# Optimization experiments

Hardware: AMD Instinct MI355X
Metric: run time of the kernel (lower is better)

The kernel has to match this reference:

```python
import jax, jax.numpy as jnp
import numpy as np

D_MODEL = 1024
N_HEADS = 16
HEAD_DIM = D_MODEL // N_HEADS
NEG = -10000.0  # module uses -10000, not -inf


def setup_inputs() -> dict:
    key = jax.random.key(0)
    ks = jax.random.split(key, 8)
    B, T = 4, 2048
    q = jax.random.normal(ks[0], (B, T, D_MODEL), dtype=jnp.float32)
    k = jax.random.normal(ks[1], (B, T, D_MODEL), dtype=jnp.float32)
    v = jax.random.normal(ks[2], (B, T, D_MODEL), dtype=jnp.float32)
    attn_mask = jnp.ones((B, T), dtype=jnp.float32)
    # xavier_uniform for square [d, d] weights: limit = sqrt(6/(d+d))
    lim = float(np.sqrt(6.0 / (D_MODEL + D_MODEL)))
    Wq = jax.random.uniform(ks[3], (D_MODEL, D_MODEL), jnp.float32, -lim, lim)
    Wk = jax.random.uniform(ks[4], (D_MODEL, D_MODEL), jnp.float32, -lim, lim)
    Wv = jax.random.uniform(ks[5], (D_MODEL, D_MODEL), jnp.float32, -lim, lim)
    Wo = jax.random.uniform(ks[6], (D_MODEL, D_MODEL), jnp.float32, -lim, lim)
    return {"q": q, "k": k, "v": v, "attn_mask": attn_mask,
            "Wq": Wq, "Wk": Wk, "Wv": Wv, "Wo": Wo, "mask_future": 1}


def _split_heads(x):
    B, T, _ = x.shape
    return x.reshape(B, T, N_HEADS, HEAD_DIM).transpose(0, 2, 1, 3)  # [B,H,T,D]


def reference(q, k, v, attn_mask, Wq, Wk, Wv, Wo, mask_future):
    # torch Linear: y = x @ W.T  (weights stored [out, in])
    qh = _split_heads(jnp.einsum('btd,ed->bte', q, Wq))
    kh = _split_heads(jnp.einsum('btd,ed->bte', k, Wk))
    vh = _split_heads(jnp.einsum('btd,ed->bte', v, Wv))
    L, S = qh.shape[-2], kh.shape[-2]
    # dual scale: each of q and k scaled by 1/d**0.25
    scale = 1.0 / jnp.sqrt(jnp.sqrt(jnp.float32(HEAD_DIM)))
    scores = jnp.einsum('bhld,bhsd->bhls', qh * scale, kh * scale)
    if mask_future:
        causal_bias = jnp.triu(jnp.full((L, S), NEG, dtype=scores.dtype), k=1)
        scores = scores + causal_bias
    # padding mask: attn_mask [B, S] -> broadcast [B,1,1,S]; 0 entries -> -10000
    pad = attn_mask[:, None, None, :]
    scores = jnp.where(pad == 0, jnp.asarray(NEG, scores.dtype), scores)
    probs = jax.nn.softmax(scores, axis=-1)  # dropout p=0.0 -> identity
    ctx = jnp.einsum('bhls,bhsd->bhld', probs, vh)
    B = ctx.shape[0]
    ctx = ctx.transpose(0, 2, 1, 3).reshape(B, L, D_MODEL)
    return jnp.einsum('btd,ed->bte', ctx, Wo)
```

## Files before the change

### kernel.cpp

```cpp
#include <hip/hip_runtime.h>

typedef unsigned short u16;
typedef __attribute__((ext_vector_type(8))) __bf16 bf16x8;
typedef __attribute__((ext_vector_type(4))) float f32x4;

#define T_SEQ 2048
#define NH 16
#define DH 64
#define DM 1024
#define NEG2 (-14426.95f)
#define QS2 (0.42466089f)

__device__ __forceinline__ u16 f2bf(float x) {
  union { float f; unsigned u; } c; c.f = x;
  unsigned r = c.u + 0x7fffu + ((c.u >> 16) & 1u);
  return (u16)(r >> 16);
}

__device__ __forceinline__ void async_load16(const void* g, void* l) {
  __builtin_amdgcn_global_load_lds(
      (const __attribute__((address_space(1))) unsigned int*)(g),
      (__attribute__((address_space(3))) unsigned int*)(l), 16, 0, 0);
}

__global__ __launch_bounds__(256) void convert_all(
    const float* __restrict__ q, const float* __restrict__ k, const float* __restrict__ v,
    const float* __restrict__ Wq, const float* __restrict__ Wk, const float* __restrict__ Wv,
    const float* __restrict__ Wo, u16* __restrict__ xb, u16* __restrict__ wb) {
  int blk = blockIdx.x;
  const float* src; u16* dst;
  if (blk < 12288) {
    int s = blk >> 12;
    src = (s == 0) ? q : (s == 1) ? k : v;
    dst = xb + (size_t)s * 8388608u;
    blk &= 4095;
  } else {
    int s = (blk - 12288) >> 9;
    src = (s == 0) ? Wq : (s == 1) ? Wk : (s == 2) ? Wv : Wo;
    dst = wb + (size_t)s * 1048576u;
    blk = (blk - 12288) & 511;
  }
  size_t base = (size_t)blk * 2048 + (size_t)threadIdx.x * 8;
  float4 a = *(const float4*)(src + base);
  float4 b2 = *(const float4*)(src + base + 4);
  u16 o[8] __attribute__((aligned(16)));
  o[0] = f2bf(a.x); o[1] = f2bf(a.y); o[2] = f2bf(a.z); o[3] = f2bf(a.w);
  o[4] = f2bf(b2.x); o[5] = f2bf(b2.y); o[6] = f2bf(b2.z); o[7] = f2bf(b2.w);
  *(uint4*)(dst + base) = *(const uint4*)o;
}

__global__ __launch_bounds__(256) void gemm_qkv(const u16* __restrict__ A,
                                                const u16* __restrict__ Wqb,
                                                const u16* __restrict__ Wkb,
                                                const u16* __restrict__ Wvb,
                                                u16* __restrict__ Qh, u16* __restrict__ Kh,
                                                u16* __restrict__ VTh) {
  __shared__ char lds[32768];
  const int tid = threadIdx.x;
  const int wid = tid >> 6, lane = tid & 63;
  const int lm = lane & 15, lq = lane >> 4;
  const int m0 = blockIdx.x * 128;
  const int n0 = blockIdx.y * 128;
  const int which = n0 >> 10;
  const int n0l = n0 & 1023;
  const u16* As = A + (size_t)which * 8388608u;
  const u16* Bw = (which == 0) ? Wqb : (which == 1) ? Wkb : Wvb;
  const int wm = wid >> 1, wn = wid & 1;
  f32x4 acc[4][4] = {};

  for (int kt = 0; kt < 1024; kt += 64) {
    __syncthreads();
    for (int i = 0; i < 4; ++i) {
      int p = wid * 4 + i;
      int mt = p >> 1, kk = p & 1;
      int col = kt + kk * 32 + lq * 8;
      async_load16(As + (size_t)(m0 + mt * 16 + lm) * 1024 + col, lds + p * 1024);
      async_load16(Bw + (size_t)(n0l + mt * 16 + lm) * 1024 + col, lds + 16384 + p * 1024);
    }
    __syncthreads();
    for (int kk = 0; kk < 2; ++kk) {
      bf16x8 af[4], bf[4];
      for (int i = 0; i < 4; ++i) {
        af[i] = *(const bf16x8*)(lds + ((wm * 4 + i) * 2 + kk) * 1024 + lane * 16);
        bf[i] = *(const bf16x8*)(lds + 16384 + ((wn * 4 + i) * 2 + kk) * 1024 + lane * 16);
      }
      for (int i = 0; i < 4; ++i)
        for (int j = 0; j < 4; ++j)
          acc[i][j] = __builtin_amdgcn_mfma_f32_16x16x32_bf16(af[i], bf[j], acc[i][j], 0, 0, 0);
    }
  }

  if (which < 2) {
    u16* O = which ? Kh : Qh;
    for (int i = 0; i < 4; ++i) {
      int row = m0 + wm * 64 + i * 16 + lq * 4;
      for (int j = 0; j < 4; ++j) {
        int nc = n0l + wn * 64 + j * 16 + lm;
        int h = nc >> 6, dh = nc & 63;
        for (int r = 0; r < 4; ++r) {
          int m = row + r;
          int b = m >> 11, t = m & 2047;
          O[(((size_t)(b * NH + h) * T_SEQ + t) << 6) + dh] = f2bf(acc[i][j][r] * QS2);
        }
      }
    }
  } else {
    for (int i = 0; i < 4; ++i) {
      int row = m0 + wm * 64 + i * 16 + lq * 4;
      int b = row >> 11, t0 = row & 2047;
      for (int j = 0; j < 4; ++j) {
        int nc = n0l + wn * 64 + j * 16 + lm;
        int h = nc >> 6, dh = nc & 63;
        u16 tmp[4] __attribute__((aligned(8)));
        for (int r = 0; r < 4; ++r) tmp[r] = f2bf(acc[i][j][r]);
        *(uint2*)(VTh + (((size_t)(b * NH + h) * DH + dh) << 11) + t0) = *(const uint2*)tmp;
      }
    }
  }
}

__global__ __launch_bounds__(256) void gemm_out(const u16* __restrict__ A,
                                                const u16* __restrict__ Bw,
                                                float* __restrict__ O) {
  __shared__ char lds[32768];
  const int tid = threadIdx.x;
  const int wid = tid >> 6, lane = tid & 63;
  const int lm = lane & 15, lq = lane >> 4;
  const int m0 = blockIdx.x * 128, n0 = blockIdx.y * 128;
  const int wm = wid >> 1, wn = wid & 1;
  f32x4 acc[4][4] = {};

  for (int kt = 0; kt < 1024; kt += 64) {
    __syncthreads();
    for (int i = 0; i < 4; ++i) {
      int p = wid * 4 + i;
      int mt = p >> 1, kk = p & 1;
      int col = kt + kk * 32 + lq * 8;
      async_load16(A + (size_t)(m0 + mt * 16 + lm) * 1024 + col, lds + p * 1024);
      async_load16(Bw + (size_t)(n0 + mt * 16 + lm) * 1024 + col, lds + 16384 + p * 1024);
    }
    __syncthreads();
    for (int kk = 0; kk < 2; ++kk) {
      bf16x8 af[4], bf[4];
      for (int i = 0; i < 4; ++i) {
        af[i] = *(const bf16x8*)(lds + ((wm * 4 + i) * 2 + kk) * 1024 + lane * 16);
        bf[i] = *(const bf16x8*)(lds + 16384 + ((wn * 4 + i) * 2 + kk) * 1024 + lane * 16);
      }
      for (int i = 0; i < 4; ++i)
        for (int j = 0; j < 4; ++j)
          acc[i][j] = __builtin_amdgcn_mfma_f32_16x16x32_bf16(af[i], bf[j], acc[i][j], 0, 0, 0);
    }
  }
  for (int i = 0; i < 4; ++i) {
    int row = m0 + wm * 64 + i * 16 + lq * 4;
    for (int j = 0; j < 4; ++j) {
      int col = n0 + wn * 64 + j * 16 + lm;
      for (int r = 0; r < 4; ++r)
        O[(size_t)(row + r) * 1024 + col] = acc[i][j][r];
    }
  }
}

__global__ __launch_bounds__(256) void attn_kernel(const u16* __restrict__ Qh,
                                                   const u16* __restrict__ Kh,
                                                   const u16* __restrict__ VTh,
                                                   const float* __restrict__ attn_mask,
                                                   const int* __restrict__ mfp,
                                                   u16* __restrict__ ctx) {
  __shared__ char kls[8192];
  __shared__ char vls[8192];
  __shared__ char pls[4][2048];
  __shared__ float maskb[T_SEQ];

  const int tid = threadIdx.x;
  const int wid = tid >> 6, lane = tid & 63;
  const int lm = lane & 15, lq = lane >> 4;
  const int bid = blockIdx.x;
  const int pr = bid & 15, h = (bid >> 4) & 15, b = bid >> 8;
  const int mf = *mfp;
  const size_t bh = (size_t)(b * NH + h);
  const u16* Qbh = Qh + bh * T_SEQ * DH;
  const u16* Kbh = Kh + bh * T_SEQ * DH;
  const u16* VTbh = VTh + bh * DH * T_SEQ;

  for (int i = tid; i < T_SEQ; i += 256)
    maskb[i] = (attn_mask[(size_t)b * T_SEQ + i] == 0.0f) ? NEG2 : 0.0f;

  for (int half = 0; half < 2; ++half) {
    const int qt = half ? (31 - pr) : pr;
    const int q0 = qt * 64;
    const int qw = q0 + wid * 16;
    bf16x8 qf[2];
    qf[0] = *(const bf16x8*)(Qbh + (size_t)(qw + lm) * DH + lq * 8);
    qf[1] = *(const bf16x8*)(Qbh + (size_t)(qw + lm) * DH + 32 + lq * 8);

    f32x4 acc[4] = {};
    float mprev = -1e30f, lsum = 0.f;

    const int nch = mf ? (qt + 1) : 32;
    for (int c = 0; c < nch; ++c) {
      const int s0 = c * 64;
      __syncthreads();
      async_load16(Kbh + (size_t)(s0 + wid * 16 + lm) * DH + lq * 8, kls + (wid * 2 + 0) * 1024);
      async_load16(Kbh + (size_t)(s0 + wid * 16 + lm) * DH + 32 + lq * 8, kls + (wid * 2 + 1) * 1024);
      async_load16(VTbh + (size_t)(wid * 16 + lm) * T_SEQ + s0 + lq * 8, vls + (wid * 2 + 0) * 1024);
      async_load16(VTbh + (size_t)(wid * 16 + lm) * T_SEQ + s0 + 32 + lq * 8, vls + (wid * 2 + 1) * 1024);
      __syncthreads();

      f32x4 sc[4];
      for (int st = 0; st < 4; ++st) {
        f32x4 z = {0.f, 0.f, 0.f, 0.f};
        sc[st] = z;
        for (int kk = 0; kk < 2; ++kk) {
          bf16x8 kf = *(const bf16x8*)(kls + ((st * 2 + kk) * 64 + lane) * 16);
          sc[st] = __builtin_amdgcn_mfma_f32_16x16x32_bf16(kf, qf[kk], sc[st], 0, 0, 0);
        }
      }
      for (int st = 0; st < 4; ++st) {
        f32x4 mb = *(const f32x4*)(maskb + s0 + st * 16 + lq * 4);
        for (int r = 0; r < 4; ++r) sc[st][r] += mb[r];
      }
      if (mf && (s0 + 64 > qw)) {
        int qg = qw + lm;
        for (int st = 0; st < 4; ++st)
          for (int r = 0; r < 4; ++r)
            if (s0 + st * 16 + lq * 4 + r > qg) sc[st][r] = NEG2;
      }
      float mx = fmaxf(fmaxf(sc[0][0], sc[0][1]), fmaxf(sc[0][2], sc[0][3]));
      for (int st = 1; st < 4; ++st) {
        float t2 = fmaxf(fmaxf(sc[st][0], sc[st][1]), fmaxf(sc[st][2], sc[st][3]));
        mx = fmaxf(mx, t2);
      }
      mx = fmaxf(mx, __shfl_xor(mx, 16));
      mx = fmaxf(mx, __shfl_xor(mx, 32));
      float mn = fmaxf(mprev, mx);
      float alpha = exp2f(mprev - mn);
      float ps = 0.f;
      for (int st = 0; st < 4; ++st)
        for (int r = 0; r < 4; ++r) {
          float p = exp2f(sc[st][r] - mn);
          sc[st][r] = p;
          ps += p;
        }
      ps += __shfl_xor(ps, 16);
      ps += __shfl_xor(ps, 32);
      lsum = lsum * alpha + ps;
      mprev = mn;
      for (int r = 0; r < 4; ++r) {
        float ar = __shfl(alpha, lq * 4 + r);
        for (int nt = 0; nt < 4; ++nt) acc[nt][r] *= ar;
      }
      {
        char* pw = pls[wid];
        for (int st = 0; st < 4; ++st) {
          int kk = st >> 1;
          int lqp = (st & 1) * 2 + (lq >> 1);
          int base = kk * 1024 + (lqp * 16 + lm) * 16 + (lq & 1) * 8;
          unsigned v0 = (unsigned)f2bf(sc[st][0]) | ((unsigned)f2bf(sc[st][1]) << 16);
          unsigned v1 = (unsigned)f2bf(sc[st][2]) | ((unsigned)f2bf(sc[st][3]) << 16);
          *(unsigned*)(pw + base) = v0;
          *(unsigned*)(pw + base + 4) = v1;
        }
      }
      asm volatile("s_waitcnt lgkmcnt(0)" ::: "memory");
      for (int kk = 0; kk < 2; ++kk) {
        bf16x8 pf = *(const bf16x8*)(pls[wid] + kk * 1024 + lane * 16);
        for (int nt = 0; nt < 4; ++nt) {
          bf16x8 vf = *(const bf16x8*)(vls + ((nt * 2 + kk) * 64 + lane) * 16);
          acc[nt] = __builtin_amdgcn_mfma_f32_16x16x32_bf16(pf, vf, acc[nt], 0, 0, 0);
        }
      }
    }
    float inv = 1.0f / lsum;
    for (int r = 0; r < 4; ++r) {
      float ir = __shfl(inv, lq * 4 + r);
      int t = qw + lq * 4 + r;
      for (int nt = 0; nt < 4; ++nt)
        ctx[((size_t)(b * T_SEQ + t) * DM) + h * DH + nt * 16 + lm] = f2bf(acc[nt][r] * ir);
    }
  }
}

extern "C" void kernel_launch(void* const* d_in, const int* in_sizes, int n_in,
                              void* d_out, int out_size, void* d_ws, size_t ws_size,
                              hipStream_t stream) {
  const float* q = (const float*)d_in[0];
  const float* k = (const float*)d_in[1];
  const float* v = (const float*)d_in[2];
  const float* attn_mask = (const float*)d_in[3];
  const float* Wq = (const float*)d_in[4];
  const float* Wk = (const float*)d_in[5];
  const float* Wv = (const float*)d_in[6];
  const float* Wo = (const float*)d_in[7];
  const int* mf = (const int*)d_in[8];

  u16* ws = (u16*)d_ws;
  u16* qb  = ws;
  u16* wqb = ws + 3u * 8388608u;
  u16* wkb = wqb + 1048576u;
  u16* wvb = wkb + 1048576u;
  u16* wob = wvb + 1048576u;
  u16* Qh  = wob + 1048576u;
  u16* Kh  = Qh + 8388608u;
  u16* VTh = Kh + 8388608u;
  u16* ctxb = ws;

  convert_all<<<14336, 256, 0, stream>>>(q, k, v, Wq, Wk, Wv, Wo, qb, wqb);

  dim3 gq(64, 24);
  gemm_qkv<<<gq, 256, 0, stream>>>(qb, wqb, wkb, wvb, Qh, Kh, VTh);

  attn_kernel<<<1024, 256, 0, stream>>>(Qh, Kh, VTh, attn_mask, mf, ctxb);

  dim3 gg(64, 8);
  gemm_out<<<gg, 256, 0, stream>>>(ctxb, wob, (float*)d_out);
}
```

Measured before the change: 399.0 us.

## Switch to fp16 MFMA, stage QKV epilogue via LDS, skip unused mask and rescale

```diff
diff --git a/kernel.cpp b/kernel.cpp
--- a/kernel.cpp
+++ b/kernel.cpp
@@ -1,7 +1,8 @@
 #include <hip/hip_runtime.h>
 
 typedef unsigned short u16;
-typedef __attribute__((ext_vector_type(8))) __bf16 bf16x8;
+typedef __attribute__((ext_vector_type(8))) _Float16 f16x8;
+typedef __attribute__((ext_vector_type(2))) __fp16 fp16v2;
 typedef __attribute__((ext_vector_type(4))) float f32x4;
 
 #define T_SEQ 2048
@@ -11,10 +12,13 @@
 #define NEG2 (-14426.95f)
 #define QS2 (0.42466089f)
 
-__device__ __forceinline__ u16 f2bf(float x) {
-  union { float f; unsigned u; } c; c.f = x;
-  unsigned r = c.u + 0x7fffu + ((c.u >> 16) & 1u);
-  return (u16)(r >> 16);
+__device__ __forceinline__ unsigned pk2(float a, float b) {
+  union { fp16v2 v; unsigned u; } c;
+  c.v = __builtin_amdgcn_cvt_pkrtz(a, b);
+  return c.u;
+}
+__device__ __forceinline__ u16 f2h(float a) {
+  union { _Float16 h; u16 u; } c; c.h = (_Float16)a; return c.u;
 }
 
 __device__ __forceinline__ void async_load16(const void* g, void* l) {
@@ -43,10 +47,10 @@
   size_t base = (size_t)blk * 2048 + (size_t)threadIdx.x * 8;
   float4 a = *(const float4*)(src + base);
   float4 b2 = *(const float4*)(src + base + 4);
-  u16 o[8] __attribute__((aligned(16)));
-  o[0] = f2bf(a.x); o[1] = f2bf(a.y); o[2] = f2bf(a.z); o[3] = f2bf(a.w);
-  o[4] = f2bf(b2.x); o[5] = f2bf(b2.y); o[6] = f2bf(b2.z); o[7] = f2bf(b2.w);
-  *(uint4*)(dst + base) = *(const uint4*)o;
+  uint4 st;
+  st.x = pk2(a.x, a.y); st.y = pk2(a.z, a.w);
+  st.z = pk2(b2.x, b2.y); st.w = pk2(b2.z, b2.w);
+  *(uint4*)(dst + base) = st;
 }
 
 __global__ __launch_bounds__(256) void gemm_qkv(const u16* __restrict__ A,
@@ -55,7 +59,7 @@
                                                 const u16* __restrict__ Wvb,
                                                 u16* __restrict__ Qh, u16* __restrict__ Kh,
                                                 u16* __restrict__ VTh) {
-  __shared__ char lds[32768];
+  __shared__ char lds[33792];
   const int tid = threadIdx.x;
   const int wid = tid >> 6, lane = tid & 63;
   const int lm = lane & 15, lq = lane >> 4;
@@ -66,6 +70,8 @@
   const u16* As = A + (size_t)which * 8388608u;
   const u16* Bw = (which == 0) ? Wqb : (which == 1) ? Wkb : Wvb;
   const int wm = wid >> 1, wn = wid & 1;
+  char* const rbase = (which < 2) ? (lds + 16384) : lds;
+  char* const cbase = (which < 2) ? lds : (lds + 16384);
   f32x4 acc[4][4] = {};
 
   for (int kt = 0; kt < 1024; kt += 64) {
@@ -79,42 +85,45 @@
     }
     __syncthreads();
     for (int kk = 0; kk < 2; ++kk) {
-      bf16x8 af[4], bf[4];
+      f16x8 rf[4], cf[4];
       for (int i = 0; i < 4; ++i) {
-        af[i] = *(const bf16x8*)(lds + ((wm * 4 + i) * 2 + kk) * 1024 + lane * 16);
-        bf[i] = *(const bf16x8*)(lds + 16384 + ((wn * 4 + i) * 2 + kk) * 1024 + lane * 16);
+        rf[i] = *(const f16x8*)(rbase + ((wm * 4 + i) * 2 + kk) * 1024 + lane * 16);
+        cf[i] = *(const f16x8*)(cbase + ((wn * 4 + i) * 2 + kk) * 1024 + lane * 16);
       }
       for (int i = 0; i < 4; ++i)
         for (int j = 0; j < 4; ++j)
-          acc[i][j] = __builtin_amdgcn_mfma_f32_16x16x32_bf16(af[i], bf[j], acc[i][j], 0, 0, 0);
-    }
-  }
-
+          acc[i][j] = __builtin_amdgcn_mfma_f32_16x16x32_f16(rf[i], cf[j], acc[i][j], 0, 0, 0);
+    }
+  }
+
+  const float s = (which < 2) ? QS2 : 1.0f;
+  __syncthreads();
+  for (int i = 0; i < 4; ++i)
+    for (int j = 0; j < 4; ++j) {
+      uint2 pv;
+      pv.x = pk2(acc[i][j][0] * s, acc[i][j][1] * s);
+      pv.y = pk2(acc[i][j][2] * s, acc[i][j][3] * s);
+      *(uint2*)(lds + (wn * 64 + j * 16 + lm) * 264 + (wm * 64 + i * 16 + lq * 4) * 2) = pv;
+    }
+  __syncthreads();
+
+  const int b = m0 >> 11, t0 = m0 & 2047, h0 = n0l >> 6;
   if (which < 2) {
     u16* O = which ? Kh : Qh;
-    for (int i = 0; i < 4; ++i) {
-      int row = m0 + wm * 64 + i * 16 + lq * 4;
-      for (int j = 0; j < 4; ++j) {
-        int nc = n0l + wn * 64 + j * 16 + lm;
-        int h = nc >> 6, dh = nc & 63;
-        for (int r = 0; r < 4; ++r) {
-          int m = row + r;
-          int b = m >> 11, t = m & 2047;
-          O[(((size_t)(b * NH + h) * T_SEQ + t) << 6) + dh] = f2bf(acc[i][j][r] * QS2);
-        }
-      }
+    for (int p = 0; p < 8; ++p) {
+      int row = p * 16 + (tid >> 4);
+      int seg = tid & 15;
+      uint4 val = *(const uint4*)(lds + row * 264 + seg * 16);
+      int hl = seg >> 3, dh0 = (seg & 7) * 8;
+      *(uint4*)(O + (((size_t)(b * NH + h0 + hl) * T_SEQ + t0 + row) << 6) + dh0) = val;
     }
   } else {
-    for (int i = 0; i < 4; ++i) {
-      int row = m0 + wm * 64 + i * 16 + lq * 4;
-      int b = row >> 11, t0 = row & 2047;
-      for (int j = 0; j < 4; ++j) {
-        int nc = n0l + wn * 64 + j * 16 + lm;
-        int h = nc >> 6, dh = nc & 63;
-        u16 tmp[4] __attribute__((aligned(8)));
-        for (int r = 0; r < 4; ++r) tmp[r] = f2bf(acc[i][j][r]);
-        *(uint2*)(VTh + (((size_t)(b * NH + h) * DH + dh) << 11) + t0) = *(const uint2*)tmp;
-      }
+    for (int p = 0; p < 8; ++p) {
+      int row = p * 16 + (tid >> 4);
+      int seg = tid & 15;
+      uint4 val = *(const uint4*)(lds + row * 264 + seg * 16);
+      int h = h0 + (row >> 6), dh = row & 63;
+      *(uint4*)(VTh + (((size_t)(b * NH + h) * DH + dh) << 11) + t0 + seg * 8) = val;
     }
   }
 }
@@ -141,14 +150,14 @@
     }
     __syncthreads();
     for (int kk = 0; kk < 2; ++kk) {
-      bf16x8 af[4], bf[4];
+      f16x8 af[4], bf[4];
       for (int i = 0; i < 4; ++i) {
-        af[i] = *(const bf16x8*)(lds + ((wm * 4 + i) * 2 + kk) * 1024 + lane * 16);
-        bf[i] = *(const bf16x8*)(lds + 16384 + ((wn * 4 + i) * 2 + kk) * 1024 + lane * 16);
+        af[i] = *(const f16x8*)(lds + ((wm * 4 + i) * 2 + kk) * 1024 + lane * 16);
+        bf[i] = *(const f16x8*)(lds + 16384 + ((wn * 4 + i) * 2 + kk) * 1024 + lane * 16);
       }
       for (int i = 0; i < 4; ++i)
         for (int j = 0; j < 4; ++j)
-          acc[i][j] = __builtin_amdgcn_mfma_f32_16x16x32_bf16(af[i], bf[j], acc[i][j], 0, 0, 0);
+          acc[i][j] = __builtin_amdgcn_mfma_f32_16x16x32_f16(af[i], bf[j], acc[i][j], 0, 0, 0);
     }
   }
   for (int i = 0; i < 4; ++i) {
@@ -171,6 +180,7 @@
   __shared__ char vls[8192];
   __shared__ char pls[4][2048];
   __shared__ float maskb[T_SEQ];
+  __shared__ int mzf;
 
   const int tid = threadIdx.x;
   const int wid = tid >> 6, lane = tid & 63;
@@ -183,16 +193,27 @@
   const u16* Kbh = Kh + bh * T_SEQ * DH;
   const u16* VTbh = VTh + bh * DH * T_SEQ;
 
-  for (int i = tid; i < T_SEQ; i += 256)
-    maskb[i] = (attn_mask[(size_t)b * T_SEQ + i] == 0.0f) ? NEG2 : 0.0f;
+  if (tid == 0) mzf = 0;
+  __syncthreads();
+  {
+    int az = 0;
+    for (int i = tid; i < T_SEQ; i += 256) {
+      float mv = attn_mask[(size_t)b * T_SEQ + i];
+      maskb[i] = (mv == 0.0f) ? NEG2 : 0.0f;
+      az |= (mv == 0.0f);
+    }
+    if (az) mzf = 1;
+  }
+  __syncthreads();
+  const int maskzero = mzf;
 
   for (int half = 0; half < 2; ++half) {
     const int qt = half ? (31 - pr) : pr;
     const int q0 = qt * 64;
     const int qw = q0 + wid * 16;
-    bf16x8 qf[2];
-    qf[0] = *(const bf16x8*)(Qbh + (size_t)(qw + lm) * DH + lq * 8);
-    qf[1] = *(const bf16x8*)(Qbh + (size_t)(qw + lm) * DH + 32 + lq * 8);
+    f16x8 qf[2];
+    qf[0] = *(const f16x8*)(Qbh + (size_t)(qw + lm) * DH + lq * 8);
+    qf[1] = *(const f16x8*)(Qbh + (size_t)(qw + lm) * DH + 32 + lq * 8);
 
     f32x4 acc[4] = {};
     float mprev = -1e30f, lsum = 0.f;
@@ -212,13 +233,15 @@
         f32x4 z = {0.f, 0.f, 0.f, 0.f};
         sc[st] = z;
         for (int kk = 0; kk < 2; ++kk) {
-          bf16x8 kf = *(const bf16x8*)(kls + ((st * 2 + kk) * 64 + lane) * 16);
-          sc[st] = __builtin_amdgcn_mfma_f32_16x16x32_bf16(kf, qf[kk], sc[st], 0, 0, 0);
-        }
-      }
-      for (int st = 0; st < 4; ++st) {
-        f32x4 mb = *(const f32x4*)(maskb + s0 + st * 16 + lq * 4);
-        for (int r = 0; r < 4; ++r) sc[st][r] += mb[r];
+          f16x8 kf = *(const f16x8*)(kls + ((st * 2 + kk) * 64 + lane) * 16);
+          sc[st] = __builtin_amdgcn_mfma_f32_16x16x32_f16(kf, qf[kk], sc[st], 0, 0, 0);
+        }
+      }
+      if (maskzero) {
+        for (int st = 0; st < 4; ++st) {
+          f32x4 mb = *(const f32x4*)(maskb + s0 + st * 16 + lq * 4);
+          for (int r = 0; r < 4; ++r) sc[st][r] += mb[r];
+        }
       }
       if (mf && (s0 + 64 > qw)) {
         int qg = qw + lm;
@@ -233,8 +256,17 @@
       }
       mx = fmaxf(mx, __shfl_xor(mx, 16));
       mx = fmaxf(mx, __shfl_xor(mx, 32));
-      float mn = fmaxf(mprev, mx);
-      float alpha = exp2f(mprev - mn);
+      float mn = mprev;
+      if (__ballot(mx > mprev) != 0ull) {
+        mn = fmaxf(mprev, mx);
+        float alpha = exp2f(mprev - mn);
+        for (int r = 0; r < 4; ++r) {
+          float ar = __shfl(alpha, lq * 4 + r);
+          for (int nt = 0; nt < 4; ++nt) acc[nt][r] *= ar;
+        }
+        lsum *= alpha;
+        mprev = mn;
+      }
       float ps = 0.f;
       for (int st = 0; st < 4; ++st)
         for (int r = 0; r < 4; ++r) {
@@ -244,30 +276,24 @@
         }
       ps += __shfl_xor(ps, 16);
       ps += __shfl_xor(ps, 32);
-      lsum = lsum * alpha + ps;
-      mprev = mn;
-      for (int r = 0; r < 4; ++r) {
-        float ar = __shfl(alpha, lq * 4 + r);
-        for (int nt = 0; nt < 4; ++nt) acc[nt][r] *= ar;
-      }
+      lsum += ps;
       {
         char* pw = pls[wid];
         for (int st = 0; st < 4; ++st) {
           int kk = st >> 1;
           int lqp = (st & 1) * 2 + (lq >> 1);
-          int base = kk * 1024 + (lqp * 16 + lm) * 16 + (lq & 1) * 8;
-          unsigned v0 = (unsigned)f2bf(sc[st][0]) | ((unsigned)f2bf(sc[st][1]) << 16);
-          unsigned v1 = (unsigned)f2bf(sc[st][2]) | ((unsigned)f2bf(sc[st][3]) << 16);
-          *(unsigned*)(pw + base) = v0;
-          *(unsigned*)(pw + base + 4) = v1;
+          uint2 pv;
+          pv.x = pk2(sc[st][0], sc[st][1]);
+          pv.y = pk2(sc[st][2], sc[st][3]);
+          *(uint2*)(pw + kk * 1024 + (lqp * 16 + lm) * 16 + (lq & 1) * 8) = pv;
         }
       }
       asm volatile("s_waitcnt lgkmcnt(0)" ::: "memory");
       for (int kk = 0; kk < 2; ++kk) {
-        bf16x8 pf = *(const bf16x8*)(pls[wid] + kk * 1024 + lane * 16);
+        f16x8 pf = *(const f16x8*)(pls[wid] + kk * 1024 + lane * 16);
         for (int nt = 0; nt < 4; ++nt) {
-          bf16x8 vf = *(const bf16x8*)(vls + ((nt * 2 + kk) * 64 + lane) * 16);
-          acc[nt] = __builtin_amdgcn_mfma_f32_16x16x32_bf16(pf, vf, acc[nt], 0, 0, 0);
+          f16x8 vf = *(const f16x8*)(vls + ((nt * 2 + kk) * 64 + lane) * 16);
+          acc[nt] = __builtin_amdgcn_mfma_f32_16x16x32_f16(pf, vf, acc[nt], 0, 0, 0);
         }
       }
     }
@@ -276,7 +302,7 @@
       float ir = __shfl(inv, lq * 4 + r);
       int t = qw + lq * 4 + r;
       for (int nt = 0; nt < 4; ++nt)
-        ctx[((size_t)(b * T_SEQ + t) * DM) + h * DH + nt * 16 + lm] = f2bf(acc[nt][r] * ir);
+        ctx[((size_t)(b * T_SEQ + t) * DM) + h * DH + nt * 16 + lm] = f2h(acc[nt][r] * ir);
     }
   }
 }
```

New measurement: 380.7 us. 4.6% less time.
